# Optimization experiments

Hardware: AMD Instinct MI355X
Metric: run time of the kernel (lower is better)

The kernel has to match this reference:

```python
import jax, jax.numpy as jnp
import numpy as np

B, S, T = 64, 1024, 64
H, A, DA, DT, P, NT = 1024, 1024, 512, 256, 256, 32
DIN = DA + A + DT  # LSTMCell input: [a_tm1_embed, att_tm1, pre_type]


def setup_inputs() -> dict:
    key = jax.random.key(0)
    ks = jax.random.split(key, 16)
    nrm = lambda k, shape, s=0.02: jax.random.normal(k, shape, jnp.float32) * s
    return {
        'src_encodings': jax.random.normal(ks[0], (B, S, H), jnp.float32),
        'W_ih': nrm(ks[1], (4 * H, DIN)), 'b_ih': jnp.zeros((4 * H,), jnp.float32),
        'W_hh': nrm(ks[2], (4 * H, H)), 'b_hh': jnp.zeros((4 * H,), jnp.float32),
        'W_att': nrm(ks[3], (H, H)),            # att_sketch_linear (no bias)
        'W_attvec': nrm(ks[4], (A, 2 * H)),     # sketch_att_vec_linear (no bias)
        'W_init': nrm(ks[5], (H, H)), 'b_init': jnp.zeros((H,), jnp.float32),  # decoder_cell_init
        'W_q2a': nrm(ks[6], (DA, A)), 'b_q2a': jnp.zeros((DA,), jnp.float32),  # query_vec_to_action_embed
        'prod_embed': nrm(ks[7], (P, DA), 0.05), 'prod_bias': jnp.zeros((P,), jnp.float32),
        'type_embed': nrm(ks[8], (NT, DT), 0.05),
        'prev_prod_ids': jax.random.randint(ks[9], (B, T), 0, P),
        'prev_type_ids': jax.random.randint(ks[10], (B, T), 0, NT),
        'target_prod_ids': jax.random.randint(ks[11], (B, T), 0, P),
        'sketch_lens': jax.random.randint(ks[12], (B,), T // 2, T + 1),
        'src_lens': jax.random.randint(ks[13], (B,), S // 2, S + 1),
    }


def _lstm_cell(x, h, c, W_ih, b_ih, W_hh, b_hh):
    gates = x @ W_ih.T + b_ih + h @ W_hh.T + b_hh
    i, f, g, o = jnp.split(gates, 4, axis=-1)
    c_new = jax.nn.sigmoid(f) * c + jax.nn.sigmoid(i) * jnp.tanh(g)
    h_new = jax.nn.sigmoid(o) * jnp.tanh(c_new)
    return h_new, c_new


def reference(src_encodings, W_ih, b_ih, W_hh, b_hh, W_att, W_attvec, W_init, b_init,
              W_q2a, b_q2a, prod_embed, prod_bias, type_embed,
              prev_prod_ids, prev_type_ids, target_prod_ids, sketch_lens, src_lens):
    Bq, Sq, Hq = src_encodings.shape
    Tq = prev_prod_ids.shape[1]
    src_valid = jnp.arange(Sq)[None, :] < src_lens[:, None]            # [B,S] True = real token
    step_valid = jnp.arange(Tq)[None, :] < sketch_lens[:, None]        # [B,T]
    prev_valid = step_valid & (jnp.arange(Tq)[None, :] > 0)            # prev action exists

    src_att = jnp.einsum('bsh,kh->bsk', src_encodings, W_att)          # att_sketch_linear
    # init_decoder_state(adaptive_avg_pool1d(enc,1))
    init_cell = src_encodings.mean(axis=1)
    h0 = jnp.tanh(init_cell @ W_init.T + b_init)
    c0 = jnp.zeros_like(h0)
    att0 = jnp.zeros((Bq, A), src_encodings.dtype)

    # precomputed grammar lookups (production / type embeddings of a_{t-1})
    a_embeds = jnp.where(prev_valid[..., None], prod_embed[prev_prod_ids], 0.0)   # [B,T,DA]
    t_embeds = jnp.where(prev_valid[..., None], type_embed[prev_type_ids], 0.0)   # [B,T,DT]
    is_first = jnp.arange(Tq) == 0                                                # [T]

    def step(carry, inp):
        h, c, att_tm1 = carry
        a_e, t_e, first = inp
        x = jnp.concatenate([a_e, att_tm1, t_e], axis=-1)
        x = jnp.where(first, 0.0, x)                                   # t==0 -> zero input
        h, c = _lstm_cell(x, h, c, W_ih, b_ih, W_hh, b_hh)
        scores = jnp.einsum('bh,bsh->bs', h, src_att)
        scores = jnp.where(src_valid, scores, -1e9)
        alpha = jax.nn.softmax(scores, axis=-1)
        ctx = jnp.einsum('bs,bsh->bh', alpha, src_encodings)
        att_t = jnp.tanh(jnp.concatenate([h, ctx], axis=-1) @ W_attvec.T)
        q = jnp.tanh(att_t @ W_q2a.T + b_q2a)                          # non_linear readout
        probs = jax.nn.softmax(q @ prod_embed.T + prod_bias, axis=-1)  # [B,P]
        return (h, c, att_t), probs

    xs = (jnp.swapaxes(a_embeds, 0, 1), jnp.swapaxes(t_embeds, 0, 1), is_first)
    _, probs = jax.lax.scan(step, (h0, c0, att0), xs)                  # [T,B,P]

    tgt = jnp.swapaxes(target_prod_ids, 0, 1)[..., None]               # [T,B,1]
    p_t = jnp.take_along_axis(probs, tgt, axis=-1)[..., 0]             # [T,B]
    logp = jnp.log(p_t + 1e-8)
    sketch_prob = jnp.sum(jnp.where(step_valid.T, logp, 0.0), axis=0)  # [B]
    return sketch_prob
```

## Files before the change

kernel.cpp:

```cpp
#include <hip/hip_runtime.h>
#include <hip/hip_bf16.h>

typedef unsigned short u16;
typedef unsigned char u8;
typedef unsigned int u32;
typedef unsigned long long u64;
typedef __attribute__((ext_vector_type(8))) short short8;
typedef __attribute__((ext_vector_type(8))) u16 ushort8;
typedef __attribute__((ext_vector_type(4))) float f32x4;
typedef __attribute__((ext_vector_type(2))) float f32x2;

__device__ __forceinline__ float bf2f(u16 x){ u32 u=((u32)x)<<16; return __builtin_bit_cast(float,u); }
__device__ __forceinline__ u16 f2bf(float f){ u32 u=__builtin_bit_cast(u32,f); u32 r=(u+0x7fffu+((u>>16)&1u))>>16; return (u16)r; }
__device__ __forceinline__ float sigf(float x){ return 1.f/(1.f+__expf(-x)); }

__device__ __forceinline__ void scf(float* p, float v){
  __hip_atomic_store(p, v, __ATOMIC_RELAXED, __HIP_MEMORY_SCOPE_AGENT);
}
__device__ __forceinline__ void scu16(u16* p, u16 v){
  __hip_atomic_store(p, v, __ATOMIC_RELAXED, __HIP_MEMORY_SCOPE_AGENT);
}
__device__ __forceinline__ int ald(const int* p){
  return __hip_atomic_load(p, __ATOMIC_RELAXED, __HIP_MEMORY_SCOPE_AGENT);
}
__device__ __forceinline__ void aadd(int* p){
  __hip_atomic_fetch_add(p, 1, __ATOMIC_RELAXED, __HIP_MEMORY_SCOPE_AGENT);
}


__global__ __launch_bounds__(256) void k_cast(const float* __restrict__ s, u16* __restrict__ d, long n){
  long i = ((long)blockIdx.x*256 + threadIdx.x)*8;
  if (i >= n) return;
  float4 a = *(const float4*)(s+i);
  float4 b = *(const float4*)(s+i+4);
  ushort8 o;
  o[0]=f2bf(a.x); o[1]=f2bf(a.y); o[2]=f2bf(a.z); o[3]=f2bf(a.w);
  o[4]=f2bf(b.x); o[5]=f2bf(b.y); o[6]=f2bf(b.z); o[7]=f2bf(b.w);
  *(ushort8*)(d+i) = o;
}

__global__ __launch_bounds__(256) void k_cast8(const float* __restrict__ s, u8* __restrict__ d, long n){
  long i = ((long)blockIdx.x*256 + threadIdx.x)*8;
  if (i >= n) return;
  float4 a = *(const float4*)(s+i);
  float4 b = *(const float4*)(s+i+4);
  u32 w0 = 0, w1 = 0;
  w0 = __builtin_amdgcn_cvt_pk_fp8_f32(a.x, a.y, w0, false);
  w0 = __builtin_amdgcn_cvt_pk_fp8_f32(a.z, a.w, w0, true);
  w1 = __builtin_amdgcn_cvt_pk_fp8_f32(b.x, b.y, w1, false);
  w1 = __builtin_amdgcn_cvt_pk_fp8_f32(b.z, b.w, w1, true);
  uint2 o; o.x = w0; o.y = w1;
  *(uint2*)(d+i) = o;
}

__global__ __launch_bounds__(256) void k_build_wc(const float* __restrict__ Wih, const float* __restrict__ Whh,
                                                  u16* __restrict__ WC){
  long i8 = (long)blockIdx.x*256 + threadIdx.x;
  if (i8 >= (long)4096*352) return;
  int j = (int)(i8/352); int kk = (int)(i8%352)*8;
  const float* src;
  if (kk < 512)        src = Wih + (long)j*1792 + kk;
  else if (kk < 768)   src = Wih + (long)j*1792 + (kk+1024);
  else if (kk < 1792)  src = Wih + (long)j*1792 + (kk-256);
  else                 src = Whh + (long)j*1024 + (kk-1792);
  u16* dst = WC + (long)j*2816 + kk;
  ushort8 o;
  #pragma unroll
  for (int q=0;q<8;++q) o[q] = f2bf(src[q]);
  *(ushort8*)dst = o;
}

__global__ __launch_bounds__(256) void k_wattT(const float* __restrict__ Wa, u16* __restrict__ WT){
  int id = blockIdx.x*256 + threadIdx.x;
  int m = id >> 10, k = id & 1023;
  WT[(long)m*1024 + k] = f2bf(Wa[(long)k*1024 + m]);
}

__global__ __launch_bounds__(256) void k_meanf(const float* __restrict__ enc, u16* __restrict__ MEANB){
  int b = blockIdx.x, h = blockIdx.y*256 + threadIdx.x;
  const float* p = enc + ((long)b<<20) + h;
  float s = 0.f;
  for (int ss=0; ss<1024; ++ss) s += p[(long)ss<<10];
  MEANB[b*1024 + h] = f2bf(s * (1.f/1024.f));
}

__global__ __launch_bounds__(256) void k_embed(const float* __restrict__ pemb, const float* __restrict__ temb,
      const int* __restrict__ pid, const int* __restrict__ tid_, const int* __restrict__ slen,
      u16* __restrict__ XC){
  int t = blockIdx.x >> 6, b = blockIdx.x & 63;
  bool valid = (t>0) && (t < slen[b]);
  int pi = pid[b*64 + t], ti = tid_[b*64 + t];
  u16* dst = XC + (long)blockIdx.x*2816;
  for (int kk = threadIdx.x; kk < 768; kk += 256){
    float v = 0.f;
    if (valid) v = (kk<512) ? pemb[(long)pi*512 + kk] : temb[(long)ti*256 + (kk-512)];
    dst[kk] = f2bf(v);
  }
}

template<int MODE>
__global__ __launch_bounds__(256) void k_gemm(const u16* __restrict__ A, long lda,
      const u16* __restrict__ W, int K, const float* __restrict__ bias,
      float* __restrict__ OF, long ldo, u16* __restrict__ OB1, long ldb1){
  int l = threadIdx.x & 63, w = threadIdx.x >> 6;
  int c = l & 15, g = l >> 4;
  int n0 = blockIdx.x*16, m0 = blockIdx.y*64;
  const u16* ap = A + (long)(m0 + w*16 + c)*lda + g*8;
  const u16* bp = W + (long)(n0 + c)*K + g*8;
  f32x4 acc = {0.f,0.f,0.f,0.f};
  int kit = K >> 5;
  #pragma unroll 4
  for (int kb=0; kb<kit; ++kb){
    short8 av = *(const short8*)(ap + kb*32);
    short8 bv = *(const short8*)(bp + kb*32);
    acc = __builtin_amdgcn_mfma_f32_16x16x32_bf16(av, bv, acc, 0, 0, 0);
  }
  #pragma unroll
  for (int r=0;r<4;++r){
    int row = m0 + w*16 + g*4 + r;
    int col = n0 + c;
    float v = acc[r];
    if (MODE==2){ OB1[(long)row*ldb1 + col] = f2bf(tanhf(v + bias[col])); }
    if (MODE==3){ OF[(long)row*ldo + col] = v + bias[col]; }
  }
}

__global__ __launch_bounds__(256) void k_loss(const float* __restrict__ LG, const int* __restrict__ tgt,
      const int* __restrict__ slen, float* __restrict__ out){
  int b = blockIdx.x;
  int w = threadIdx.x >> 6, l = threadIdx.x & 63;
  int len = slen[b];
  float accum = 0.f;
  for (int t = w; t < 64; t += 4){
    if (t >= len) continue;
    const float* lp = LG + ((long)(t*64 + b))*256;
    float v0=lp[l], v1=lp[l+64], v2=lp[l+128], v3=lp[l+192];
    float mx = fmaxf(fmaxf(v0,v1), fmaxf(v2,v3));
    #pragma unroll
    for (int off=32; off; off>>=1) mx = fmaxf(mx, __shfl_xor(mx, off));
    float s = __expf(v0-mx)+__expf(v1-mx)+__expf(v2-mx)+__expf(v3-mx);
    #pragma unroll
    for (int off=32; off; off>>=1) s += __shfl_xor(s, off);
    float ltg = lp[tgt[b*64 + t]];
    float p = __expf(ltg - mx)/s;
    accum += logf(p + 1e-8f);
  }
  __shared__ float sm[4];
  if (l == 0) sm[w] = accum;
  __syncthreads();
  if (threadIdx.x == 0) out[b] = sm[0]+sm[1]+sm[2]+sm[3];
}


__global__ __launch_bounds__(1024,1) void k_decoder(
      const u8* __restrict__ ENC8, const u16* __restrict__ WC,
      const u16* __restrict__ WAVT, const u16* __restrict__ WAVEC,
      const float* __restrict__ bih, const float* __restrict__ bhh,
      u16* __restrict__ XC, u16* __restrict__ ATT,
      float* __restrict__ HWT, float* __restrict__ PLT,
      u16* __restrict__ CTXBT, u16* __restrict__ CTXFT,
      const int* __restrict__ src_lens, int* __restrict__ BAR){
  const int tid = threadIdx.x;
  const int w = tid >> 6, l = tid & 63, c = l & 15, g = l >> 4;
  const int bx = blockIdx.x;

  __shared__ float smem[12320];
  f32x4* lacc  = (f32x4*)smem;
  float* s_ctx = smem;
  float* s_ls  = smem + 12288;
  u16*   ldsc  = (u16*)smem;
  f32x4* lacc4 = (f32x4*)(smem + 8192);

  int* F1  = BAR;
  int* F4  = BAR + 256;
  int* F2  = BAR + 512;
  int* F3  = BAR + 576;
  int* F3c = BAR + 640;

  const int n0 = bx << 2;
  const int jrow = n0 + (c & 3) + ((c >> 2) << 10);
  const float biasj = bih[jrow] + bhh[jrow];
  const int kh = w >> 2, mt = w & 3;
  const int lbase = l & 0x33;
  float creg[4] = {0.f,0.f,0.f,0.f};
  const int mt2 = bx & 3, nt2 = bx >> 2;
  const int b3 = bx >> 2, ci3 = bx & 3;
  int len3 = src_lens[b3]; if (len3 < 1) len3 = 1; if (len3 > 1024) len3 = 1024;
  const int chunk3 = (len3 + 3) >> 2;
  int s0 = ci3*chunk3;
  int s1 = s0 + chunk3; if (s1 > len3) s1 = len3;
  const u8* encb = ENC8 + (((long)b3)<<20);
  int lim = s1 - s0 - w;
  int nqv = (lim <= 0) ? 0 : ((lim + 15) >> 4);
  if (nqv > 16) nqv = 16;
  const int mt4 = bx & 3, nt4 = bx >> 2;
  const int grp = bx & 15;

  uint4 er[12];
  #pragma unroll
  for (int q=0;q<12;++q){
    int r = s0 + q*16 + w;
    if (r >= s1) r = s0;
    er[q] = *(const uint4*)(encb + ((long)r<<10) + l*16);
  }

  for (int t = 0; t < 64; ++t){
    const int gen = t + 1;
    const u16* XCt = XC + (size_t)t*64*2816;
    u16* XCn = XC + (size_t)(t+1)*64*2816;
    const u16* Hcur = XCn + 1792;
    float* HW   = HWT  + ((size_t)t<<16);
    float* PL   = PLT  + ((size_t)t<<8);
    u16*  CTXB  = CTXBT + ((size_t)t<<18);
    u16*  CTXF  = CTXFT + ((size_t)t<<16);

    {
      const u16* ap = XCt + (long)(mt*16 + c)*2816 + kh*704 + g*8;
      const u16* bp = WC  + (long)jrow*2816 + kh*704 + g*8;
      f32x4 acc = {0.f,0.f,0.f,0.f};
      #pragma unroll 11
      for (int kb=0; kb<22; ++kb){
        short8 av = *(const short8*)(ap + kb*32);
        short8 bv = *(const short8*)(bp + kb*32);
        acc = __builtin_amdgcn_mfma_f32_16x16x32_bf16(av, bv, acc, 0, 0, 0);
      }
      lacc[w*64 + l] = acc;
      __syncthreads();
      if (w < 4){
        f32x4 a0 = lacc[w*64 + l];
        f32x4 a1 = lacc[(w+4)*64 + l];
        f32x4 a2 = lacc[(w+8)*64 + l];
        f32x4 a3 = lacc[(w+12)*64 + l];
        #pragma unroll
        for (int r=0;r<4;++r){
          float val = a0[r] + a1[r] + a2[r] + a3[r] + biasj;
          float iv = __shfl(val, lbase);
          float fv = __shfl(val, lbase+4);
          float gv = __shfl(val, lbase+8);
          float ov = __shfl(val, lbase+12);
          if ((l & 12) == 0){
            float cn = sigf(fv)*creg[r] + sigf(iv)*tanhf(gv);
            float hn = sigf(ov)*tanhf(cn);
            creg[r] = cn;
            int b = w*16 + g*4 + r;
            int n = n0 + (l & 3);
            scu16(XCn + (long)b*2816 + 1792 + n, f2bf(hn));
          }
        }
      }
    }
    __syncthreads();
    if (tid == 0) aadd(F1 + grp*16);
    if (tid < 64){
      const int* pf = F1 + (tid & 15)*16;
      int tgt = gen*16;
      for(;;){
        int v = ald(pf);
        if (__all(v >= tgt)) break;
        __builtin_amdgcn_s_sleep(1);
      }
    }
    __syncthreads();

    {
      const u16* ap = Hcur + (long)(mt2*16 + c)*2816 + w*64 + g*8;
      const u16* bp = WAVT + (long)(nt2*16 + c)*1024 + w*64 + g*8;
      f32x4 acc = {0.f,0.f,0.f,0.f};
      #pragma unroll
      for (int kb=0; kb<2; ++kb){
        short8 av = *(const short8*)(ap + kb*32);
        short8 bv = *(const short8*)(bp + kb*32);
        acc = __builtin_amdgcn_mfma_f32_16x16x32_bf16(av, bv, acc, 0, 0, 0);
      }
      lacc[w*64 + l] = acc;
      __syncthreads();
      if (w == 0){
        f32x4 rd = lacc[l];
        #pragma unroll
        for (int w2=1; w2<16; ++w2) rd += lacc[w2*64 + l];
        #pragma unroll
        for (int r=0;r<4;++r)
          scf(HW + (long)(mt2*16 + g*4 + r)*1024 + nt2*16 + c, rd[r]);
      }
    }
    __syncthreads();
    if (tid == 0){
      aadd(F2 + mt2*16);
      while (ald(F2 + (bx>>6)*16) < gen*64) __builtin_amdgcn_s_sleep(1);
    }
    __syncthreads();

    {
      float hw[16], ctx[16];
      const float* hwp = HW + b3*1024 + l*16;
      #pragma unroll
      for (int jj=0;jj<4;++jj){
        float4 v = *(const float4*)(hwp + jj*4);
        hw[4*jj]=v.x; hw[4*jj+1]=v.y; hw[4*jj+2]=v.z; hw[4*jj+3]=v.w;
      }
      #pragma unroll
      for (int jj=0;jj<16;++jj) ctx[jj]=0.f;
      float lsum = 0.f;
      auto proc = [&](uint4 ev){
        float e[16];
        #pragma unroll
        for (int jj=0;jj<4;++jj){
          u32 x = ((const u32*)&ev)[jj];
          f32x2 lo = __builtin_amdgcn_cvt_pk_f32_fp8(x, false);
          f32x2 hi = __builtin_amdgcn_cvt_pk_f32_fp8(x, true);
          e[4*jj]=lo[0]; e[4*jj+1]=lo[1]; e[4*jj+2]=hi[0]; e[4*jj+3]=hi[1];
        }
        float sc = 0.f;
        #pragma unroll
        for (int jj=0;jj<16;++jj) sc += e[jj]*hw[jj];
        #pragma unroll
        for (int off=32; off; off>>=1) sc += __shfl_xor(sc, off);
        float pe = __expf(sc);
        lsum += pe;
        #pragma unroll
        for (int jj=0;jj<16;++jj) ctx[jj] += pe*e[jj];
      };
      #pragma unroll
      for (int q=0;q<12;++q) if (q < nqv) proc(er[q]);
      for (int q=12; q<nqv; ++q){
        uint4 ev = *(const uint4*)(encb + ((long)(s0 + q*16 + w)<<10) + l*16);
        proc(ev);
      }
      if (l == 0) s_ls[w] = lsum;
      if (w < 8){
        #pragma unroll
        for (int jj=0;jj<16;++jj) s_ctx[w*1024 + l*16 + jj] = ctx[jj];
      }
      __syncthreads();
      if (w >= 8){
        #pragma unroll
        for (int jj=0;jj<16;++jj) s_ctx[(w-8)*1024 + l*16 + jj] += ctx[jj];
      }
      __syncthreads();
      {
        float v = 0.f;
        #pragma unroll
        for (int p=0;p<8;++p) v += s_ctx[p*1024 + tid];
        scu16(CTXB + (((long)bx)<<10) + tid, f2bf(v));
      }
      if (tid == 0){
        float L = 0.f;
        #pragma unroll
        for (int q=0;q<16;++q) L += s_ls[q];
        scf(PL + bx, L);
      }
    }
    __syncthreads();
    if (tid == 0) aadd(F3 + (bx>>6)*16);

    if (bx < 64){
      if (tid == 0){
        while (ald(F3 + (bx>>4)*16) < gen*64) __builtin_amdgcn_s_sleep(1);
      }
      __syncthreads();
      int b = bx;
      float L = PL[b*4] + PL[b*4+1] + PL[b*4+2] + PL[b*4+3];
      float inv = (L > 0.f) ? 1.f/L : 0.f;
      const u16* c0 = CTXB + (long)(b*4+0)*1024;
      const u16* c1 = CTXB + (long)(b*4+1)*1024;
      const u16* c2 = CTXB + (long)(b*4+2)*1024;
      const u16* c3 = CTXB + (long)(b*4+3)*1024;
      float v = bf2f(c0[tid]) + bf2f(c1[tid]) + bf2f(c2[tid]) + bf2f(c3[tid]);
      scu16(CTXF + (long)b*1024 + tid, f2bf(v*inv));
      __syncthreads();
      if (tid == 0) aadd(F3c + (bx>>4)*16);
    }
    if (tid == 0){
      while (ald(F3c + mt4*16) < gen*16) __builtin_amdgcn_s_sleep(1);
    }
    __syncthreads();

    {
      const int b16 = w;
      const u16* cf = CTXF + (long)(mt4*16 + b16)*1024;
      ushort8 v0 = *(const ushort8*)(cf + l*8);
      ushort8 v1 = *(const ushort8*)(cf + (l+64)*8);
      const int swz = (b16 & 7) << 3;
      *(ushort8*)(ldsc + ((b16*1024 + l*8) ^ swz)) = v0;
      *(ushort8*)(ldsc + ((b16*1024 + (l+64)*8) ^ swz)) = v1;
      __syncthreads();
      f32x4 acc = {0.f,0.f,0.f,0.f};
      const int koff = (w < 8) ? w*128 : 1024 + (w-8)*128;
      const u16* bp = WAVEC + (long)(nt4*16 + c)*2048 + koff + g*8;
      if (w < 8){
        const u16* ap = Hcur + (long)(mt4*16 + c)*2816 + w*128 + g*8;
        #pragma unroll
        for (int kb=0; kb<4; ++kb){
          short8 av = *(const short8*)(ap + kb*32);
          short8 bv = *(const short8*)(bp + kb*32);
          acc = __builtin_amdgcn_mfma_f32_16x16x32_bf16(av, bv, acc, 0, 0, 0);
        }
      } else {
        const int cswz = (c & 7) << 3;
        const int kbase = c*1024 + (w-8)*128 + g*8;
        #pragma unroll
        for (int kb=0; kb<4; ++kb){
          short8 av = *(const short8*)(ldsc + ((kbase + kb*32) ^ cswz));
          short8 bv = *(const short8*)(bp + kb*32);
          acc = __builtin_amdgcn_mfma_f32_16x16x32_bf16(av, bv, acc, 0, 0, 0);
        }
      }
      lacc4[w*64 + l] = acc;
      __syncthreads();
      if (w == 0){
        f32x4 rd = lacc4[l];
        #pragma unroll
        for (int w2=1; w2<16; ++w2) rd += lacc4[w2*64 + l];
        #pragma unroll
        for (int r=0;r<4;++r){
          int b_ = mt4*16 + g*4 + r;
          int col = nt4*16 + c;
          u16 x = f2bf(tanhf(rd[r]));
          scu16(XCn + (long)b_*2816 + 768 + col, x);
          ATT[((long)t*64 + b_)*1024 + col] = x;
        }
      }
    }
    __syncthreads();
    if (tid == 0) aadd(F4 + grp*16);
    if (tid < 64){
      const int* pf = F4 + (tid & 15)*16;
      int tgt = gen*16;
      for(;;){
        int v = ald(pf);
        if (__all(v >= tgt)) break;
        __builtin_amdgcn_s_sleep(1);
      }
    }
    __syncthreads();
  }
}

extern "C" void kernel_launch(void* const* d_in, const int* in_sizes, int n_in,
                              void* d_out, int out_size, void* d_ws, size_t ws_size,
                              hipStream_t stream){
  const float* enc      = (const float*)d_in[0];
  const float* W_ih     = (const float*)d_in[1];
  const float* b_ih     = (const float*)d_in[2];
  const float* W_hh     = (const float*)d_in[3];
  const float* b_hh     = (const float*)d_in[4];
  const float* W_att    = (const float*)d_in[5];
  const float* W_attvec = (const float*)d_in[6];
  const float* W_init   = (const float*)d_in[7];
  const float* b_init   = (const float*)d_in[8];
  const float* W_q2a    = (const float*)d_in[9];
  const float* b_q2a    = (const float*)d_in[10];
  const float* prod_emb = (const float*)d_in[11];
  const float* prod_bias= (const float*)d_in[12];
  const float* type_emb = (const float*)d_in[13];
  const int* prev_pid   = (const int*)d_in[14];
  const int* prev_tid   = (const int*)d_in[15];
  const int* target     = (const int*)d_in[16];
  const int* sk_lens    = (const int*)d_in[17];
  const int* src_lens   = (const int*)d_in[18];
  float* out = (float*)d_out;

  char* ws = (char*)d_ws;
  size_t o = 0;
  auto alloc = [&](size_t bytes)->char*{ char* p = ws + o; o += (bytes + 255) & ~(size_t)255; return p; };
  u8*   ENC8 = (u8*)alloc((size_t)64*1024*1024);
  u16*  WC   = (u16*)alloc((size_t)4096*2816*2);
  u16*  WAVT = (u16*)alloc((size_t)1024*1024*2);
  u16*  WAVEC= (u16*)alloc((size_t)1024*2048*2);
  u16*  WQ   = (u16*)alloc((size_t)512*1024*2);
  u16*  PE   = (u16*)alloc((size_t)256*512*2);
  u16*  WINIT= (u16*)alloc((size_t)1024*1024*2);
  u16*  MEANB= (u16*)alloc((size_t)64*1024*2);
  u16*  XC   = (u16*)alloc((size_t)65*64*2816*2);
  u16*  ATT  = (u16*)alloc((size_t)64*64*1024*2);
  float* HWT = (float*)alloc((size_t)64*64*1024*4);
  float* PLT = (float*)alloc((size_t)64*256*4);
  u16*  CTXBT=(u16*)alloc((size_t)64*256*1024*2);
  u16*  CTXFT=(u16*)alloc((size_t)64*64*1024*2);
  u16*  Q    = (u16*)alloc((size_t)4096*512*2);
  float* LG  = (float*)alloc((size_t)4096*256*4);
  int*  BAR  = (int*)alloc(4096);
  (void)ws_size; (void)in_sizes; (void)n_in; (void)out_size;

  hipMemsetAsync(XC, 0, (size_t)64*2816*2, stream);
  hipMemsetAsync(BAR, 0, 4096, stream);

  k_cast8<<<32768,256,0,stream>>>(enc, ENC8, (long)64*1024*1024);
  k_cast<<<1024,256,0,stream>>>(W_attvec, WAVEC, (long)1024*2048);
  k_cast<<<256,256,0,stream>>>(W_q2a, WQ, (long)512*1024);
  k_cast<<<64,256,0,stream>>>(prod_emb, PE, (long)256*512);
  k_cast<<<512,256,0,stream>>>(W_init, WINIT, (long)1024*1024);
  k_build_wc<<<5632,256,0,stream>>>(W_ih, W_hh, WC);
  k_wattT<<<4096,256,0,stream>>>(W_att, WAVT);
  k_meanf<<<dim3(64,4),256,0,stream>>>(enc, MEANB);
  k_gemm<2><<<dim3(64,1),256,0,stream>>>(MEANB, 1024L, WINIT, 1024, b_init,
                                         nullptr, 0L, XC + 1792, 2816L);
  k_embed<<<4096,256,0,stream>>>(prod_emb, type_emb, prev_pid, prev_tid, sk_lens, XC);

  k_decoder<<<256,1024,0,stream>>>(ENC8, WC, WAVT, WAVEC, b_ih, b_hh,
                                   XC, ATT, HWT, PLT, CTXBT, CTXFT, src_lens, BAR);

  k_gemm<2><<<dim3(32,64),256,0,stream>>>(ATT, 1024L, WQ, 1024, b_q2a,
                                          nullptr, 0L, Q, 512L);
  k_gemm<3><<<dim3(16,64),256,0,stream>>>(Q, 512L, PE, 512, prod_bias,
                                          LG, 256L, nullptr, 0L);
  k_loss<<<64,256,0,stream>>>(LG, target, sk_lens, out);
}
```

Baseline: 4.493 ms.

## Replace per-phase flag spins with unified hierarchical grid barrier and fold ctx reduce

Replaces the assorted per-phase flag/counter synchronizations in the persistent decoder with a single two-level grid barrier (16 group counters feeding a root counter that broadcasts a generation to 16 release flags). The separate ctx-normalization stage (64 blocks writing CTXF plus an extra barrier) is removed: every block now sums the four partial CTXB slices itself while filling LDS. This cuts one synchronization round per timestep and the CTXF buffer, at the cost of redundant reads of the partial contexts and making each barrier a full-grid wait where some were previously partial.

```diff
diff --git a/kernel.cpp b/kernel.cpp
--- a/kernel.cpp
+++ b/kernel.cpp
@@ -22,9 +22,6 @@
 }
 __device__ __forceinline__ int ald(const int* p){
   return __hip_atomic_load(p, __ATOMIC_RELAXED, __HIP_MEMORY_SCOPE_AGENT);
-}
-__device__ __forceinline__ void aadd(int* p){
-  __hip_atomic_fetch_add(p, 1, __ATOMIC_RELAXED, __HIP_MEMORY_SCOPE_AGENT);
 }
 
 
@@ -151,6 +148,20 @@
   if (threadIdx.x == 0) out[b] = sm[0]+sm[1]+sm[2]+sm[3];
 }
 
+__device__ __forceinline__ void gbar(int* __restrict__ BAR, int gen){
+  int grp = blockIdx.x & 15;
+  int prev = __hip_atomic_fetch_add(BAR + grp*16, 1, __ATOMIC_RELAXED, __HIP_MEMORY_SCOPE_AGENT);
+  if (prev == gen*16 - 1){
+    int p2 = __hip_atomic_fetch_add(BAR + 256, 1, __ATOMIC_RELAXED, __HIP_MEMORY_SCOPE_AGENT);
+    if (p2 == gen*16 - 1){
+      #pragma unroll
+      for (int i=0;i<16;++i)
+        __hip_atomic_store(BAR + 320 + i*16, gen, __ATOMIC_RELAXED, __HIP_MEMORY_SCOPE_AGENT);
+    }
+  }
+  while (ald(BAR + 320 + grp*16) < gen)
+    __builtin_amdgcn_s_sleep(2);
+}
 
 __global__ __launch_bounds__(1024,1) void k_decoder(
       const u8* __restrict__ ENC8, const u16* __restrict__ WC,
@@ -158,11 +169,12 @@
       const float* __restrict__ bih, const float* __restrict__ bhh,
       u16* __restrict__ XC, u16* __restrict__ ATT,
       float* __restrict__ HWT, float* __restrict__ PLT,
-      u16* __restrict__ CTXBT, u16* __restrict__ CTXFT,
-      const int* __restrict__ src_lens, int* __restrict__ BAR){
+      u16* __restrict__ CTXBT, const int* __restrict__ src_lens,
+      int* __restrict__ BAR){
   const int tid = threadIdx.x;
   const int w = tid >> 6, l = tid & 63, c = l & 15, g = l >> 4;
   const int bx = blockIdx.x;
+  int genb = 0;
 
   __shared__ float smem[12320];
   f32x4* lacc  = (f32x4*)smem;
@@ -170,12 +182,6 @@
   float* s_ls  = smem + 12288;
   u16*   ldsc  = (u16*)smem;
   f32x4* lacc4 = (f32x4*)(smem + 8192);
-
-  int* F1  = BAR;
-  int* F4  = BAR + 256;
-  int* F2  = BAR + 512;
-  int* F3  = BAR + 576;
-  int* F3c = BAR + 640;
 
   const int n0 = bx << 2;
   const int jrow = n0 + (c & 3) + ((c >> 2) << 10);
@@ -194,7 +200,7 @@
   int nqv = (lim <= 0) ? 0 : ((lim + 15) >> 4);
   if (nqv > 16) nqv = 16;
   const int mt4 = bx & 3, nt4 = bx >> 2;
-  const int grp = bx & 15;
+  const int b16 = tid >> 6, lane64 = tid & 63;
 
   uint4 er[12];
   #pragma unroll
@@ -205,14 +211,12 @@
   }
 
   for (int t = 0; t < 64; ++t){
-    const int gen = t + 1;
     const u16* XCt = XC + (size_t)t*64*2816;
     u16* XCn = XC + (size_t)(t+1)*64*2816;
     const u16* Hcur = XCn + 1792;
     float* HW   = HWT  + ((size_t)t<<16);
     float* PL   = PLT  + ((size_t)t<<8);
     u16*  CTXB  = CTXBT + ((size_t)t<<18);
-    u16*  CTXF  = CTXFT + ((size_t)t<<16);
 
     {
       const u16* ap = XCt + (long)(mt*16 + c)*2816 + kh*704 + g*8;
@@ -249,17 +253,9 @@
         }
       }
     }
-    __syncthreads();
-    if (tid == 0) aadd(F1 + grp*16);
-    if (tid < 64){
-      const int* pf = F1 + (tid & 15)*16;
-      int tgt = gen*16;
-      for(;;){
-        int v = ald(pf);
-        if (__all(v >= tgt)) break;
-        __builtin_amdgcn_s_sleep(1);
-      }
-    }
+    ++genb;
+    __syncthreads();
+    if (tid == 0) gbar(BAR, genb);
     __syncthreads();
 
     {
@@ -283,11 +279,9 @@
           scf(HW + (long)(mt2*16 + g*4 + r)*1024 + nt2*16 + c, rd[r]);
       }
     }
-    __syncthreads();
-    if (tid == 0){
-      aadd(F2 + mt2*16);
-      while (ald(F2 + (bx>>6)*16) < gen*64) __builtin_amdgcn_s_sleep(1);
-    }
+    ++genb;
+    __syncthreads();
+    if (tid == 0) gbar(BAR, genb);
     __syncthreads();
 
     {
@@ -350,39 +344,33 @@
         scf(PL + bx, L);
       }
     }
-    __syncthreads();
-    if (tid == 0) aadd(F3 + (bx>>6)*16);
-
-    if (bx < 64){
-      if (tid == 0){
-        while (ald(F3 + (bx>>4)*16) < gen*64) __builtin_amdgcn_s_sleep(1);
-      }
-      __syncthreads();
-      int b = bx;
+    ++genb;
+    __syncthreads();
+    if (tid == 0) gbar(BAR, genb);
+    __syncthreads();
+
+    {
+      int b = mt4*16 + b16;
       float L = PL[b*4] + PL[b*4+1] + PL[b*4+2] + PL[b*4+3];
       float inv = (L > 0.f) ? 1.f/L : 0.f;
-      const u16* c0 = CTXB + (long)(b*4+0)*1024;
-      const u16* c1 = CTXB + (long)(b*4+1)*1024;
-      const u16* c2 = CTXB + (long)(b*4+2)*1024;
-      const u16* c3 = CTXB + (long)(b*4+3)*1024;
-      float v = bf2f(c0[tid]) + bf2f(c1[tid]) + bf2f(c2[tid]) + bf2f(c3[tid]);
-      scu16(CTXF + (long)b*1024 + tid, f2bf(v*inv));
-      __syncthreads();
-      if (tid == 0) aadd(F3c + (bx>>4)*16);
-    }
-    if (tid == 0){
-      while (ald(F3c + mt4*16) < gen*16) __builtin_amdgcn_s_sleep(1);
-    }
-    __syncthreads();
-
-    {
-      const int b16 = w;
-      const u16* cf = CTXF + (long)(mt4*16 + b16)*1024;
-      ushort8 v0 = *(const ushort8*)(cf + l*8);
-      ushort8 v1 = *(const ushort8*)(cf + (l+64)*8);
+      const u16* r0 = CTXB + (long)(b*4+0)*1024;
+      const u16* r1 = CTXB + (long)(b*4+1)*1024;
+      const u16* r2 = CTXB + (long)(b*4+2)*1024;
+      const u16* r3 = CTXB + (long)(b*4+3)*1024;
       const int swz = (b16 & 7) << 3;
-      *(ushort8*)(ldsc + ((b16*1024 + l*8) ^ swz)) = v0;
-      *(ushort8*)(ldsc + ((b16*1024 + (l+64)*8) ^ swz)) = v1;
+      #pragma unroll
+      for (int q=0;q<2;++q){
+        int mcol8 = (lane64 + q*64)*8;
+        ushort8 v0 = *(const ushort8*)(r0 + mcol8);
+        ushort8 v1 = *(const ushort8*)(r1 + mcol8);
+        ushort8 v2 = *(const ushort8*)(r2 + mcol8);
+        ushort8 v3 = *(const ushort8*)(r3 + mcol8);
+        ushort8 o;
+        #pragma unroll
+        for (int j=0;j<8;++j)
+          o[j] = f2bf((bf2f(v0[j]) + bf2f(v1[j]) + bf2f(v2[j]) + bf2f(v3[j])) * inv);
+        *(ushort8*)(ldsc + ((b16*1024 + mcol8) ^ swz)) = o;
+      }
       __syncthreads();
       f32x4 acc = {0.f,0.f,0.f,0.f};
       const int koff = (w < 8) ? w*128 : 1024 + (w-8)*128;
@@ -421,17 +409,9 @@
         }
       }
     }
-    __syncthreads();
-    if (tid == 0) aadd(F4 + grp*16);
-    if (tid < 64){
-      const int* pf = F4 + (tid & 15)*16;
-      int tgt = gen*16;
-      for(;;){
-        int v = ald(pf);
-        if (__all(v >= tgt)) break;
-        __builtin_amdgcn_s_sleep(1);
-      }
-    }
+    ++genb;
+    __syncthreads();
+    if (tid == 0) gbar(BAR, genb);
     __syncthreads();
   }
 }
@@ -476,7 +456,6 @@
   float* HWT = (float*)alloc((size_t)64*64*1024*4);
   float* PLT = (float*)alloc((size_t)64*256*4);
   u16*  CTXBT=(u16*)alloc((size_t)64*256*1024*2);
-  u16*  CTXFT=(u16*)alloc((size_t)64*64*1024*2);
   u16*  Q    = (u16*)alloc((size_t)4096*512*2);
   float* LG  = (float*)alloc((size_t)4096*256*4);
   int*  BAR  = (int*)alloc(4096);
@@ -498,7 +477,7 @@
   k_embed<<<4096,256,0,stream>>>(prod_emb, type_emb, prev_pid, prev_tid, sk_lens, XC);
 
   k_decoder<<<256,1024,0,stream>>>(ENC8, WC, WAVT, WAVEC, b_ih, b_hh,
-                                   XC, ATT, HWT, PLT, CTXBT, CTXFT, src_lens, BAR);
+                                   XC, ATT, HWT, PLT, CTXBT, src_lens, BAR);
 
   k_gemm<2><<<dim3(32,64),256,0,stream>>>(ATT, 1024L, WQ, 1024, b_q2a,
                                           nullptr, 0L, Q, 512L);
```

Result: faster. 3.868 ms (-13.9%).
